# Optimization experiments

Measured on AMD Instinct MI355X. Metric: run time of the kernel, lower is better.

The kernel has to match this reference:

```python
import jax, jax.numpy as jnp
import numpy as np

D_MODEL = 1024
NUM_HEADS = 16
HEAD_DIM = D_MODEL // NUM_HEADS


def setup_inputs() -> dict:
    key = jax.random.key(0)
    ks = jax.random.split(key, 5)
    s = 0.02
    x = jax.random.normal(ks[0], (4, 2048, D_MODEL), dtype=jnp.float32)
    W_Q = jax.random.normal(ks[1], (D_MODEL, D_MODEL), dtype=jnp.float32) * s
    W_K = jax.random.normal(ks[2], (D_MODEL, D_MODEL), dtype=jnp.float32) * s
    W_V = jax.random.normal(ks[3], (D_MODEL, D_MODEL), dtype=jnp.float32) * s
    W_O = jax.random.normal(ks[4], (D_MODEL, D_MODEL), dtype=jnp.float32) * s
    return {"x": x, "W_Q": W_Q, "W_K": W_K, "W_V": W_V, "W_O": W_O}


def reference(x, W_Q, W_K, W_V, W_O):
    b, s, d = x.shape
    h, hd = NUM_HEADS, HEAD_DIM
    scale = 1.0 / np.sqrt(hd).astype(np.float32)
    # nn.Linear applies x @ W.T; split heads then transpose -> (b, h, s, hd)
    def split(W):
        return (x @ W.T).reshape(b, s, h, hd).transpose(0, 2, 1, 3)
    Q, K, V = split(W_Q), split(W_K), split(W_V)
    scores = jnp.einsum('bhqd,bhkd->bhqk', Q, K) * scale
    causal = jnp.triu(jnp.ones((s, s), dtype=bool), k=1)
    scores = jnp.where(causal, -jnp.inf, scores)
    weights = jax.nn.softmax(scores, axis=-1)
    ctx = jnp.einsum('bhqk,bhkd->bhqd', weights, V)
    ctx = ctx.transpose(0, 2, 1, 3).reshape(b, s, d)
    return ctx @ W_O.T
```

## Files before the change

### kernel.cpp

```cpp
#include <hip/hip_runtime.h>


#define B_  4
#define S_  2048
#define D_  1024
#define H_  16
#define HD_ 64

typedef __attribute__((ext_vector_type(8))) short bf16x8;
typedef __attribute__((ext_vector_type(4))) float f32x4;

#define MFMA16 __builtin_amdgcn_mfma_f32_16x16x32_bf16

__device__ __forceinline__ unsigned short f2b(float f) {
  unsigned u = __builtin_bit_cast(unsigned, f);
  unsigned r = (u + 0x7FFFu + ((u >> 16) & 1u)) >> 16;
  return (unsigned short)r;
}

__device__ __forceinline__ unsigned cvtpk(float lo, float hi) {
  unsigned r;
  asm("v_cvt_pk_bf16_f32 %0, %1, %2" : "=v"(r) : "v"(lo), "v"(hi));
  return r;
}

__device__ __forceinline__ void gll16(const void* g, const void* l) {
  __builtin_amdgcn_global_load_lds(
      (const __attribute__((address_space(1))) unsigned int*)g,
      (__attribute__((address_space(3))) unsigned int*)l, 16, 0, 0);
}

__global__ __launch_bounds__(256) void cvt_all(
    const float4* __restrict__ x,  const float4* __restrict__ wq,
    const float4* __restrict__ wk, const float4* __restrict__ wv,
    const float4* __restrict__ wo,
    ushort4* __restrict__ xb,  ushort4* __restrict__ wqb,
    ushort4* __restrict__ wkb, ushort4* __restrict__ wvb,
    ushort4* __restrict__ wob)
{
  const int y = blockIdx.y;
  const float4* in; ushort4* out;
  if (y < 8)       { in = x  + (size_t)y * 262144; out = xb  + (size_t)y * 262144; }
  else if (y == 8) { in = wq; out = wqb; }
  else if (y == 9) { in = wk; out = wkb; }
  else if (y == 10){ in = wv; out = wvb; }
  else             { in = wo; out = wob; }
  int i = blockIdx.x * 256 + threadIdx.x;
  float4 v = in[i];
  ushort4 o;
  o.x = f2b(v.x); o.y = f2b(v.y); o.z = f2b(v.z); o.w = f2b(v.w);
  out[i] = o;
}

#define GSTG(BF, K0) { \
    _Pragma("unroll") for (int t = 0; t < 2; ++t) { \
      const int grow_ = t*64 + w*16 + srow; \
      const int lbas_ = (t*256 + w*64) * 8; \
      gll16(A + (size_t)(arow + grow_)*1024 + (K0) + scol, &As[BF][lbas_]); \
      gll16(W + (size_t)(brow + grow_)*1024 + (K0) + scol, &Bs[BF][lbas_]); } }

#define GSTEP(BF, SW) { \
    bf16x8 af[4], bfr[4]; \
    _Pragma("unroll") for (int i = 0; i < 4; ++i) \
      af[i]  = *(const bf16x8*)(&As[BF][(wm*64 + i*16 + r16)*32 + g*8]); \
    _Pragma("unroll") for (int i = 0; i < 4; ++i) \
      bfr[i] = *(const bf16x8*)(&Bs[BF][(wn*64 + i*16 + r16)*32 + g*8]); \
    _Pragma("unroll") for (int i = 0; i < 4; ++i) \
      _Pragma("unroll") for (int j = 0; j < 4; ++j) \
        acc[i][j] = (SW) ? MFMA16(bfr[j], af[i], acc[i][j], 0, 0, 0) \
                         : MFMA16(af[i], bfr[j], acc[i][j], 0, 0, 0); }

#define GLOOP(SW) \
  for (int kt = 0; kt < 32; kt += 2) { \
    __syncthreads(); \
    GSTG(1, (kt + 1) * 32); \
    GSTEP(0, SW); \
    __syncthreads(); \
    if (kt + 2 < 32) GSTG(0, (kt + 2) * 32); \
    GSTEP(1, SW); \
  }

template<int MODE>
__global__ __launch_bounds__(256) void gemm_bt(
    const unsigned short* __restrict__ A,
    const unsigned short* __restrict__ W,
    unsigned short* __restrict__ OQ,
    unsigned short* __restrict__ OK,
    unsigned short* __restrict__ OV,
    float* __restrict__ OF)
{
  const int tid  = threadIdx.x;
  const int lane = tid & 63;
  const int w    = tid >> 6;
  const int wm   = w >> 1, wn = w & 1;
  const int r16  = lane & 15, g = lane >> 4;

  const int orig = blockIdx.x + 64 * blockIdx.y;
  const int t_   = orig >> 3;
  const int bm   = (orig & 7) * 8 + (t_ & 7);
  const int bn   = t_ >> 3;

  __shared__ unsigned short As[2][4096];
  __shared__ unsigned short Bs[2][4096];

  const int arow = bm * 128, brow = bn * 128;
  const int srow = lane >> 2, scol = (lane & 3) * 8;

  f32x4 acc[4][4] = {};
  const bool vblk = (MODE == 0) && (bn >= 16);
  GSTG(0, 0);
  if (!vblk) { GLOOP(true) } else { GLOOP(false) }

  if (MODE == 1) {
    #pragma unroll
    for (int i = 0; i < 4; ++i)
      #pragma unroll
      for (int j = 0; j < 4; ++j) {
        int t = arow + wm*64 + i*16 + r16;
        int f = brow + wn*64 + j*16 + g*4;
        float4 st;
        st.x = acc[i][j][0]; st.y = acc[i][j][1];
        st.z = acc[i][j][2]; st.w = acc[i][j][3];
        *(float4*)(&OF[(size_t)t * 1024 + f]) = st;
      }
  } else if (!vblk) {
    unsigned short* Od = (bn < 8) ? OQ : OK;
    const float scl = (bn < 8) ? 0.18033688f : 1.0f;
    #pragma unroll
    for (int i = 0; i < 4; ++i)
      #pragma unroll
      for (int j = 0; j < 4; ++j) {
        int t = arow + wm*64 + i*16 + r16;
        int f = (brow & 1023) + wn*64 + j*16 + g*4;
        int b = t >> 11, s = t & 2047, h = f >> 6, hd = f & 63;
        uint2 cw;
        cw.x = cvtpk(acc[i][j][0] * scl, acc[i][j][1] * scl);
        cw.y = cvtpk(acc[i][j][2] * scl, acc[i][j][3] * scl);
        *(uint2*)(&Od[((((size_t)b*H_ + h)*S_) + s)*HD_ + hd]) = cw;
      }
  } else {
    #pragma unroll
    for (int i = 0; i < 4; ++i)
      #pragma unroll
      for (int j = 0; j < 4; ++j) {
        int t0 = arow + wm*64 + i*16 + g*4;
        int f  = (brow & 1023) + wn*64 + j*16 + r16;
        int b = t0 >> 11, s = t0 & 2047, h = f >> 6, hd = f & 63;
        uint2 cw;
        cw.x = cvtpk(acc[i][j][0], acc[i][j][1]);
        cw.y = cvtpk(acc[i][j][2], acc[i][j][3]);
        *(uint2*)(&OV[(((size_t)b*H_ + h)*HD_ + hd)*S_ + s]) = cw;
      }
  }
}

#define ASTG(BF, KB) { \
    gll16(Kh + (size_t)((KB) + tr0 +     rsub)*HD_ + csw, &KVb[BF][0][ tr0     *64]); \
    gll16(Kh + (size_t)((KB) + tr0 + 8 + rsub)*HD_ + csw, &KVb[BF][0][(tr0 + 8)*64]); \
    gll16(Vh + (size_t)(tr0 +     rsub)*S_ + (KB) + csw,  &KVb[BF][1][ tr0     *64]); \
    gll16(Vh + (size_t)(tr0 + 8 + rsub)*S_ + (KB) + csw,  &KVb[BF][1][(tr0 + 8)*64]); }

#define ACOMP(BF, KB) { \
    const int kb_ = (KB); \
    if (kb_ <= qw) { \
      f32x4 sc[4]; \
      __builtin_amdgcn_s_setprio(1); \
      _Pragma("unroll") for (int c = 0; c < 4; ++c) { \
        bf16x8 kf0 = *(const bf16x8*)((const char*)&KVb[BF][0][0] + (c*16 + r16)*128 + ((( g      ^ (r16 & 7)) & 7) << 4)); \
        bf16x8 kf1 = *(const bf16x8*)((const char*)&KVb[BF][0][0] + (c*16 + r16)*128 + ((((4 + g) ^ (r16 & 7)) & 7) << 4)); \
        f32x4 s_ = {}; \
        s_ = MFMA16(kf0, qf[0], s_, 0, 0, 0); \
        s_ = MFMA16(kf1, qf[1], s_, 0, 0, 0); \
        sc[c] = s_; } \
      __builtin_amdgcn_s_setprio(0); \
      f32x4 p4[4]; \
      if (kb_ + 63 > qw) { \
        const int qrow_ = qw + r16; \
        _Pragma("unroll") for (int c = 0; c < 4; ++c) \
          _Pragma("unroll") for (int r = 0; r < 4; ++r) \
            p4[c][r] = (kb_ + c*16 + g*4 + r > qrow_) ? 0.f : exp2f(sc[c][r]); \
      } else { \
        _Pragma("unroll") for (int c = 0; c < 4; ++c) \
          _Pragma("unroll") for (int r = 0; r < 4; ++r) \
            p4[c][r] = exp2f(sc[c][r]); } \
      { char* prp_ = Plw + r16*128; \
        const int swz_ = (r16 & 7) << 4; \
        _Pragma("unroll") for (int c = 0; c < 4; ++c) { \
          uint2 pw_; \
          pw_.x = cvtpk(p4[c][0], p4[c][1]); \
          pw_.y = cvtpk(p4[c][2], p4[c][3]); \
          *(uint2*)(prp_ + ((c*32 + g*8) ^ swz_)) = pw_; } } \
      __builtin_amdgcn_s_setprio(1); \
      _Pragma("unroll") for (int kc = 0; kc < 2; ++kc) { \
        bf16x8 pf_ = *(const bf16x8*)(Plw + r16*128 + ((kc*64 + g*16) ^ ((r16 & 7) << 4))); \
        oL = MFMA16(onesf, pf_, oL, 0, 0, 0); \
        _Pragma("unroll") for (int dn = 0; dn < 4; ++dn) { \
          bf16x8 vf_ = *(const bf16x8*)((const char*)&KVb[BF][1][0] + (dn*16 + r16)*128 + ((((kc*4 + g) ^ (r16 & 7)) & 7) << 4)); \
          oT[dn] = MFMA16(vf_, pf_, oT[dn], 0, 0, 0); } } \
      __builtin_amdgcn_s_setprio(0); \
    } }

__global__ __launch_bounds__(256, 4) void attn_fwd(
    const unsigned short* __restrict__ Q,
    const unsigned short* __restrict__ K,
    const unsigned short* __restrict__ Vt,
    unsigned short* __restrict__ C)
{
  const int tid  = threadIdx.x;
  const int lane = tid & 63;
  const int w    = tid >> 6;
  const int r16  = lane & 15, g = lane >> 4;

  const int l_   = blockIdx.x;
  const int bh   = (l_ & 7) * 8 + ((l_ >> 3) & 7);
  const int px   = l_ >> 6;
  const int bb   = bh >> 4, hh = bh & 15;

  const unsigned short* Qh = Q  + (size_t)bh * S_ * HD_;
  const unsigned short* Kh = K  + (size_t)bh * S_ * HD_;
  const unsigned short* Vh = Vt + (size_t)bh * HD_ * S_;

  __shared__ unsigned short KVb[2][2][4096];
  __shared__ unsigned short Pl[4][1024];
  char* Plw = (char*)&Pl[w][0];

  const int rsub = lane >> 3;
  const int csw  = ((lane & 7) ^ rsub) * 8;
  const int tr0  = w * 16;

  bf16x8 onesf;
  #pragma unroll
  for (int j = 0; j < 8; ++j) onesf[j] = (short)0x3F80;

  ASTG(0, 0);

  #pragma unroll
  for (int ph = 0; ph < 2; ++ph) {
    const int jt = ph ? (31 - px) : px;
    const int q0 = jt * 64;
    const int qw = q0 + w * 16;
    const int nt = (jt + 2) & ~1;

    bf16x8 qf[2];
    #pragma unroll
    for (int dh = 0; dh < 2; ++dh)
      qf[dh] = *(const bf16x8*)(&Qh[(size_t)(qw + r16) * HD_ + dh*32 + g*8]);

    f32x4 oT[4] = {};
    f32x4 oL = {};

    for (int kt = 0; kt < nt; kt += 2) {
      __syncthreads();
      ASTG(1, (kt + 1) * 64);
      ACOMP(0, kt * 64);
      __syncthreads();
      if (kt + 2 < nt)      { ASTG(0, (kt + 2) * 64); }
      else if (ph == 0)     { ASTG(0, 0); }
      ACOMP(1, (kt + 1) * 64);
    }

    float inv = 1.0f / oL[0];
    int tok = bb * S_ + qw + r16;
    #pragma unroll
    for (int dn = 0; dn < 4; ++dn) {
      uint2 cw;
      cw.x = cvtpk(oT[dn][0] * inv, oT[dn][1] * inv);
      cw.y = cvtpk(oT[dn][2] * inv, oT[dn][3] * inv);
      *(uint2*)(&C[(size_t)tok * D_ + hh*HD_ + dn*16 + g*4]) = cw;
    }
  }
}

extern "C" void kernel_launch(void* const* d_in, const int* in_sizes, int n_in,
                              void* d_out, int out_size, void* d_ws, size_t ws_size,
                              hipStream_t stream) {
  const float* x  = (const float*)d_in[0];
  const float* Wq = (const float*)d_in[1];
  const float* Wk = (const float*)d_in[2];
  const float* Wv = (const float*)d_in[3];
  const float* Wo = (const float*)d_in[4];

  char* ws = (char*)d_ws;
  unsigned short* xb  = (unsigned short*)(ws);
  unsigned short* Wqb = (unsigned short*)(ws + 16777216);
  unsigned short* Wkb = (unsigned short*)(ws + 18874368);
  unsigned short* Wvb = (unsigned short*)(ws + 20971520);
  unsigned short* Wob = (unsigned short*)(ws + 23068672);
  unsigned short* Qb  = (unsigned short*)(ws + 25165824);
  unsigned short* Kb  = (unsigned short*)(ws + 41943040);
  unsigned short* Vtb = (unsigned short*)(ws + 58720256);
  unsigned short* Cb  = (unsigned short*)(ws + 75497472);

  cvt_all<<<dim3(1024, 12), 256, 0, stream>>>(
      (const float4*)x, (const float4*)Wq, (const float4*)Wk,
      (const float4*)Wv, (const float4*)Wo,
      (ushort4*)xb, (ushort4*)Wqb, (ushort4*)Wkb, (ushort4*)Wvb, (ushort4*)Wob);

  gemm_bt<0><<<dim3(64, 24), 256, 0, stream>>>(xb, Wqb, Qb, Kb, Vtb, nullptr);
  attn_fwd<<<1024, 256, 0, stream>>>(Qb, Kb, Vtb, Cb);
  gemm_bt<1><<<dim3(64, 8), 256, 0, stream>>>(Cb, Wob, nullptr, nullptr, nullptr,
                                              (float*)d_out);
}
```

Before: 178.0 us.

## Process 128-query tiles per block with two 16-row query groups per wave

The attention kernel now gives each block a 128-query tile, with each wave handling 32 query rows as two 16-row groups. This replaces the earlier scheme of two 64-query phases (px and 31-px) per block. Each K/V tile staged in shared memory is reused across twice as many queries, which halves K/V load traffic per query. The cost is that causal load balancing now relies on scheduling the heaviest tiles first (jt = 15 - ...) instead of pairing tiles. Register pressure is higher, launch bounds drop to 3 blocks per CU, and the P staging buffer doubles.

```diff
diff --git a/kernel.cpp b/kernel.cpp
--- a/kernel.cpp
+++ b/kernel.cpp
@@ -160,30 +160,32 @@
     gll16(Vh + (size_t)(tr0 +     rsub)*S_ + (KB) + csw,  &KVb[BF][1][ tr0     *64]); \
     gll16(Vh + (size_t)(tr0 + 8 + rsub)*S_ + (KB) + csw,  &KVb[BF][1][(tr0 + 8)*64]); }
 
-#define ACOMP(BF, KB) { \
+#define ACOMP2(BF, KB) { \
     const int kb_ = (KB); \
-    if (kb_ <= qw) { \
-      f32x4 sc[4]; \
+    if (kb_ <= qw + 31) { \
+      f32x4 sc[2][4]; \
       __builtin_amdgcn_s_setprio(1); \
       _Pragma("unroll") for (int c = 0; c < 4; ++c) { \
         bf16x8 kf0 = *(const bf16x8*)((const char*)&KVb[BF][0][0] + (c*16 + r16)*128 + ((( g      ^ (r16 & 7)) & 7) << 4)); \
         bf16x8 kf1 = *(const bf16x8*)((const char*)&KVb[BF][0][0] + (c*16 + r16)*128 + ((((4 + g) ^ (r16 & 7)) & 7) << 4)); \
-        f32x4 s_ = {}; \
-        s_ = MFMA16(kf0, qf[0], s_, 0, 0, 0); \
-        s_ = MFMA16(kf1, qf[1], s_, 0, 0, 0); \
-        sc[c] = s_; } \
+        _Pragma("unroll") for (int qi = 0; qi < 2; ++qi) { \
+          f32x4 s_ = {}; \
+          s_ = MFMA16(kf0, qf[qi][0], s_, 0, 0, 0); \
+          s_ = MFMA16(kf1, qf[qi][1], s_, 0, 0, 0); \
+          sc[qi][c] = s_; } } \
       __builtin_amdgcn_s_setprio(0); \
-      f32x4 p4[4]; \
-      if (kb_ + 63 > qw) { \
-        const int qrow_ = qw + r16; \
-        _Pragma("unroll") for (int c = 0; c < 4; ++c) \
-          _Pragma("unroll") for (int r = 0; r < 4; ++r) \
-            p4[c][r] = (kb_ + c*16 + g*4 + r > qrow_) ? 0.f : exp2f(sc[c][r]); \
-      } else { \
-        _Pragma("unroll") for (int c = 0; c < 4; ++c) \
-          _Pragma("unroll") for (int r = 0; r < 4; ++r) \
-            p4[c][r] = exp2f(sc[c][r]); } \
-      { char* prp_ = Plw + r16*128; \
+      _Pragma("unroll") for (int qi = 0; qi < 2; ++qi) { \
+        f32x4 p4[4]; \
+        if (kb_ + 63 > qw + qi*16) { \
+          const int qrow_ = qw + qi*16 + r16; \
+          _Pragma("unroll") for (int c = 0; c < 4; ++c) \
+            _Pragma("unroll") for (int r = 0; r < 4; ++r) \
+              p4[c][r] = (kb_ + c*16 + g*4 + r > qrow_) ? 0.f : exp2f(sc[qi][c][r]); \
+        } else { \
+          _Pragma("unroll") for (int c = 0; c < 4; ++c) \
+            _Pragma("unroll") for (int r = 0; r < 4; ++r) \
+              p4[c][r] = exp2f(sc[qi][c][r]); } \
+        char* prp_ = Plw + (qi*16 + r16)*128; \
         const int swz_ = (r16 & 7) << 4; \
         _Pragma("unroll") for (int c = 0; c < 4; ++c) { \
           uint2 pw_; \
@@ -192,15 +194,18 @@
           *(uint2*)(prp_ + ((c*32 + g*8) ^ swz_)) = pw_; } } \
       __builtin_amdgcn_s_setprio(1); \
       _Pragma("unroll") for (int kc = 0; kc < 2; ++kc) { \
-        bf16x8 pf_ = *(const bf16x8*)(Plw + r16*128 + ((kc*64 + g*16) ^ ((r16 & 7) << 4))); \
-        oL = MFMA16(onesf, pf_, oL, 0, 0, 0); \
+        bf16x8 pf0_ = *(const bf16x8*)(Plw + r16*128        + ((kc*64 + g*16) ^ ((r16 & 7) << 4))); \
+        bf16x8 pf1_ = *(const bf16x8*)(Plw + (16 + r16)*128 + ((kc*64 + g*16) ^ ((r16 & 7) << 4))); \
+        oL[0] = MFMA16(onesf, pf0_, oL[0], 0, 0, 0); \
+        oL[1] = MFMA16(onesf, pf1_, oL[1], 0, 0, 0); \
         _Pragma("unroll") for (int dn = 0; dn < 4; ++dn) { \
           bf16x8 vf_ = *(const bf16x8*)((const char*)&KVb[BF][1][0] + (dn*16 + r16)*128 + ((((kc*4 + g) ^ (r16 & 7)) & 7) << 4)); \
-          oT[dn] = MFMA16(vf_, pf_, oT[dn], 0, 0, 0); } } \
+          oT[0][dn] = MFMA16(vf_, pf0_, oT[0][dn], 0, 0, 0); \
+          oT[1][dn] = MFMA16(vf_, pf1_, oT[1][dn], 0, 0, 0); } } \
       __builtin_amdgcn_s_setprio(0); \
     } }
 
-__global__ __launch_bounds__(256, 4) void attn_fwd(
+__global__ __launch_bounds__(256, 3) void attn_fwd(
     const unsigned short* __restrict__ Q,
     const unsigned short* __restrict__ K,
     const unsigned short* __restrict__ Vt,
@@ -213,7 +218,7 @@
 
   const int l_   = blockIdx.x;
   const int bh   = (l_ & 7) * 8 + ((l_ >> 3) & 7);
-  const int px   = l_ >> 6;
+  const int jt   = 15 - (l_ >> 6);
   const int bb   = bh >> 4, hh = bh & 15;
 
   const unsigned short* Qh = Q  + (size_t)bh * S_ * HD_;
@@ -221,7 +226,7 @@
   const unsigned short* Vh = Vt + (size_t)bh * HD_ * S_;
 
   __shared__ unsigned short KVb[2][2][4096];
-  __shared__ unsigned short Pl[4][1024];
+  __shared__ unsigned short Pl[4][2048];
   char* Plw = (char*)&Pl[w][0];
 
   const int rsub = lane >> 3;
@@ -232,40 +237,40 @@
   #pragma unroll
   for (int j = 0; j < 8; ++j) onesf[j] = (short)0x3F80;
 
+  const int q0 = jt * 128;
+  const int qw = q0 + w * 32;
+  const int nt = 2 * jt + 2;
+
+  bf16x8 qf[2][2];
+  #pragma unroll
+  for (int qi = 0; qi < 2; ++qi)
+    #pragma unroll
+    for (int dh = 0; dh < 2; ++dh)
+      qf[qi][dh] = *(const bf16x8*)(&Qh[(size_t)(qw + qi*16 + r16) * HD_ + dh*32 + g*8]);
+
+  f32x4 oT[2][4] = {};
+  f32x4 oL[2] = {};
+
   ASTG(0, 0);
 
+  for (int kt = 0; kt < nt; kt += 2) {
+    __syncthreads();
+    ASTG(1, (kt + 1) * 64);
+    ACOMP2(0, kt * 64);
+    __syncthreads();
+    if (kt + 2 < nt) ASTG(0, (kt + 2) * 64);
+    ACOMP2(1, (kt + 1) * 64);
+  }
+
   #pragma unroll
-  for (int ph = 0; ph < 2; ++ph) {
-    const int jt = ph ? (31 - px) : px;
-    const int q0 = jt * 64;
-    const int qw = q0 + w * 16;
-    const int nt = (jt + 2) & ~1;
-
-    bf16x8 qf[2];
-    #pragma unroll
-    for (int dh = 0; dh < 2; ++dh)
-      qf[dh] = *(const bf16x8*)(&Qh[(size_t)(qw + r16) * HD_ + dh*32 + g*8]);
-
-    f32x4 oT[4] = {};
-    f32x4 oL = {};
-
-    for (int kt = 0; kt < nt; kt += 2) {
-      __syncthreads();
-      ASTG(1, (kt + 1) * 64);
-      ACOMP(0, kt * 64);
-      __syncthreads();
-      if (kt + 2 < nt)      { ASTG(0, (kt + 2) * 64); }
-      else if (ph == 0)     { ASTG(0, 0); }
-      ACOMP(1, (kt + 1) * 64);
-    }
-
-    float inv = 1.0f / oL[0];
-    int tok = bb * S_ + qw + r16;
+  for (int qi = 0; qi < 2; ++qi) {
+    float inv = 1.0f / oL[qi][0];
+    int tok = bb * S_ + qw + qi*16 + r16;
     #pragma unroll
     for (int dn = 0; dn < 4; ++dn) {
       uint2 cw;
-      cw.x = cvtpk(oT[dn][0] * inv, oT[dn][1] * inv);
-      cw.y = cvtpk(oT[dn][2] * inv, oT[dn][3] * inv);
+      cw.x = cvtpk(oT[qi][dn][0] * inv, oT[qi][dn][1] * inv);
+      cw.y = cvtpk(oT[qi][dn][2] * inv, oT[qi][dn][3] * inv);
       *(uint2*)(&C[(size_t)tok * D_ + hh*HD_ + dn*16 + g*4]) = cw;
     }
   }
```

New measurement: 170.1 us. -4.5%, faster.
